# Optimization experiments

Hardware: AMD Instinct MI355X
Metric: run time of the kernel (lower is better)

The kernel has to match this reference:

```python
import jax, jax.numpy as jnp
import numpy as np

EMBED_DIM = 2048
NUM_HEADS = 16
HEAD_DIM = EMBED_DIM // NUM_HEADS
BATCH, SEQ = 4, 4096


def setup_inputs() -> dict:
    key = jax.random.key(0)
    k1, k2, k3, k4 = jax.random.split(key, 4)
    scale = 1.0 / np.sqrt(EMBED_DIM)
    x = jax.random.normal(k1, (BATCH, SEQ, EMBED_DIM), dtype=jnp.float32)
    W_qkv = jax.random.normal(k2, (EMBED_DIM, 3 * EMBED_DIM), dtype=jnp.float32) * scale
    W_out = jax.random.normal(k3, (EMBED_DIM, EMBED_DIM), dtype=jnp.float32) * scale
    b_out = jax.random.normal(k4, (EMBED_DIM,), dtype=jnp.float32) * 0.01
    return {"x": x, "W_qkv": W_qkv, "W_out": W_out, "b_out": b_out}


def reference(x, W_qkv, W_out, b_out):
    b, s, _ = x.shape
    # qkv: (b, s, 3, h, d)
    qkv = (x @ W_qkv).reshape(b, s, 3, NUM_HEADS, HEAD_DIM)
    q, k, v = qkv[:, :, 0], qkv[:, :, 1], qkv[:, :, 2]
    # NOTE: faithful to source — scores mix HEADS per token: (b, s, h, h)
    scores = jnp.einsum('bshd,bsHd->bshH', q, k) / jnp.sqrt(jnp.float32(HEAD_DIM))
    w = jax.nn.softmax(scores, axis=-1)
    attn = jnp.einsum('bshH,bsHd->bshd', w, v).reshape(b, s, EMBED_DIM)
    return attn @ W_out + b_out
```

## Files before the change

### kernel.cpp

```cpp
#include <hip/hip_runtime.h>
#include <hip/hip_bf16.h>
#include <cstdint>


#define TOKENS 16384
#define EMB    2048
#define NQKV   6144

typedef __bf16 bf16x8_t __attribute__((ext_vector_type(8)));
typedef float  f32x4_t  __attribute__((ext_vector_type(4)));

#define GLOAD16(gsrc, ldst)                                                    \
  __builtin_amdgcn_global_load_lds(                                            \
      (const __attribute__((address_space(1))) void*)(uintptr_t)(gsrc),        \
      (__attribute__((address_space(3))) void*)(uint32_t)(uintptr_t)(ldst),    \
      16, 0, 0)

static __device__ __forceinline__ unsigned short f32_to_bf16_bits(float f) {
  union { float f; uint32_t u; } x; x.f = f;
  uint32_t u = x.u;
  u += 0x7fffu + ((u >> 16) & 1u);
  return (unsigned short)(u >> 16);
}

__global__ __launch_bounds__(256) void cvt_f32_bf16(
    const float4* __restrict__ in, ushort4* __restrict__ out, int n4) {
  const int stride = gridDim.x * blockDim.x;
  for (int i = blockIdx.x * blockDim.x + threadIdx.x; i < n4; i += stride) {
    float4 v = in[i];
    ushort4 o;
    o.x = f32_to_bf16_bits(v.x);
    o.y = f32_to_bf16_bits(v.y);
    o.z = f32_to_bf16_bits(v.z);
    o.w = f32_to_bf16_bits(v.w);
    out[i] = o;
  }
}

__global__ __launch_bounds__(256) void transpose_cvt(
    const float* __restrict__ in, unsigned short* __restrict__ out, int R, int C) {
  __shared__ float tile[32][33];
  const int bx = blockIdx.x * 32;
  const int by = blockIdx.y * 32;
  const int tx = threadIdx.x;
  const int ty = threadIdx.y;
#pragma unroll
  for (int j = 0; j < 32; j += 8)
    tile[ty + j][tx] = in[(size_t)(by + ty + j) * C + bx + tx];
  __syncthreads();
#pragma unroll
  for (int j = 0; j < 32; j += 8)
    out[(size_t)(bx + ty + j) * R + by + tx] = f32_to_bf16_bits(tile[tx][ty + j]);
}

template <bool OUT_BF16>
__global__ __launch_bounds__(512, 1) void gemm_bt(
    const unsigned short* __restrict__ A,
    const unsigned short* __restrict__ BT,
    unsigned short* __restrict__ Cb,
    float* __restrict__ Cf,
    const float* __restrict__ bias,
    int M, int N) {
  constexpr int K = 2048;
  constexpr int BK = 64;
  constexpr int NKT = K / BK;
  __shared__ __align__(16) char lds[131072];

  const int nbx = N / 256;
  const int nwg = gridDim.x;
  const int bid = blockIdx.x;
  const int swzb = (bid & 7) * (nwg >> 3) + (bid >> 3);
  const int by = swzb / nbx;
  const int bx = swzb % nbx;

  const int t    = threadIdx.x;
  const int lane = t & 63;
  const int wid  = t >> 6;
  const int wr   = wid >> 2;
  const int wc   = wid & 3;
  const int lr   = lane & 15;
  const int g    = lane >> 4;

  const unsigned short* aSrc = A  + (size_t)by * 256 * K;
  const unsigned short* bSrc = BT + (size_t)bx * 256 * K;

  int aoff[2], boff[2];
#pragma unroll
  for (int i = 0; i < 2; ++i) {
    const int p   = (i * 512 + t) * 16;
    const int lo  = p ^ (((p >> 7) & 7) << 4);
    const int rih = lo >> 7;
    const int kbe = (lo & 127) >> 1;
    aoff[i] = (((rih >> 6) << 7) + (rih & 63)) * K + kbe;
    boff[i] = (((rih >> 5) << 6) + (rih & 31)) * K + kbe;
  }
  const int ldst = wid << 10;

  auto stageA = [&](int h, int k0, char* bufA) {
#pragma unroll
    for (int i = 0; i < 2; ++i)
      GLOAD16(aSrc + aoff[i] + h * (64 * K) + k0, bufA + h * 16384 + i * 8192 + ldst);
  };
  auto stageB = [&](int h, int k0, char* bufB) {
#pragma unroll
    for (int i = 0; i < 2; ++i)
      GLOAD16(bSrc + boff[i] + h * (32 * K) + k0, bufB + h * 16384 + i * 8192 + ldst);
  };

  const int sw   = (lr & 7) << 4;
  const int col0 = (g * 16) ^ sw;
  const int col1 = (64 + g * 16) ^ sw;
  const int aRow = (wr * 64 + lr) * 128;
  const int bRow = (wc * 32 + lr) * 128;

  f32x4_t acc[8][4] = {};
  bf16x8_t av0[4][2], av1[4][2];
  bf16x8_t bv0[2][2], bv1[2][2];

#define LDA_INTO(dst, bufA_, q)                                                \
  {                                                                            \
    const char* _b = (bufA_) + (q) * 16384 + aRow;                             \
    _Pragma("unroll") for (int m2 = 0; m2 < 4; ++m2) {                         \
      dst[m2][0] = *(const bf16x8_t*)(_b + m2 * 2048 + col0);                  \
      dst[m2][1] = *(const bf16x8_t*)(_b + m2 * 2048 + col1);                  \
    }                                                                          \
  }
#define LDB_INTO(dst, bufB_, pair)                                             \
  {                                                                            \
    _Pragma("unroll") for (int e = 0; e < 2; ++e) {                            \
      const int nf = (pair) * 2 + e;                                           \
      const char* _b = (bufB_) + (nf >> 1) * 16384 + (nf & 1) * 2048 + bRow;   \
      dst[e][0] = *(const bf16x8_t*)(_b + col0);                               \
      dst[e][1] = *(const bf16x8_t*)(_b + col1);                               \
    }                                                                          \
  }
#define MFMAQ(AV, BV, Q, PAIR)                                                 \
  _Pragma("unroll") for (int m2 = 0; m2 < 4; ++m2)                             \
  _Pragma("unroll") for (int e = 0; e < 2; ++e)                                \
  _Pragma("unroll") for (int ks = 0; ks < 2; ++ks)                             \
    acc[(Q) * 4 + m2][(PAIR) * 2 + e] = __builtin_amdgcn_mfma_f32_16x16x32_bf16( \
        AV[m2][ks], BV[e][ks], acc[(Q) * 4 + m2][(PAIR) * 2 + e], 0, 0, 0);

#define SBR __builtin_amdgcn_sched_barrier(0)
#define TAIL(NN)                                                               \
  SBR; __builtin_amdgcn_s_barrier();                                           \
  asm volatile("s_waitcnt lgkmcnt(" #NN ")" ::: "memory");                     \
  SBR; __builtin_amdgcn_s_setprio(1);
#define PEND                                                                   \
  __builtin_amdgcn_s_setprio(0); SBR; __builtin_amdgcn_s_barrier();
#define VMC(NN) asm volatile("s_waitcnt vmcnt(" #NN ")" ::: "memory"); SBR;

#define BODY(KT, S1, S2, VM3, VM4, T4)                                         \
  {                                                                            \
    char* cA = lds + ((KT) & 1) * 65536;                                       \
    char* cB = cA + 32768;                                                     \
    char* nA = lds + (((KT) + 1) & 1) * 65536;                                 \
    char* nB = nA + 32768;                                                     \
    const int k2 = ((KT) + 2) * BK;                                            \
      \
    LDB_INTO(bv1, cB, 1); SBR;                                                 \
    TAIL(4);                                                                   \
    MFMAQ(av0, bv0, 0, 0);                                                     \
    LDA_INTO(av1, cA, 1);                                                      \
    PEND;                                                                      \
                               \
    if (S2) { stageA(0, k2, cA); } SBR;                                        \
    TAIL(8);                                                                   \
    MFMAQ(av0, bv1, 0, 1);                                                     \
    PEND;                                                                      \
                                         \
    VMC(VM3);                                                                  \
    if (S2) { stageB(0, k2, cB); } SBR;                                        \
    TAIL(0);                                                                   \
    MFMAQ(av1, bv1, 1, 1);                                                     \
    PEND;                                                                      \
                             \
    VMC(VM4);                                                                  \
    if (S2) { stageA(1, k2, cA); stageB(1, k2, cB); } SBR;                     \
    if (S1) { LDA_INTO(av0, nA, 0); } SBR;                                     \
    TAIL(T4);                                                                  \
    MFMAQ(av1, bv0, 1, 0);                                                     \
    if (S1) { LDB_INTO(bv0, nB, 0); }                                          \
    PEND;                                                                      \
  }

  {
    char* b0A = lds;
    char* b0B = lds + 32768;
    char* b1A = lds + 65536;
    char* b1B = b1A + 32768;
    stageA(0, 0, b0A); stageA(1, 0, b0A);
    stageB(0, 0, b0B); stageB(1, 0, b0B);
    stageA(0, BK, b1A);
    stageB(0, BK, b1B);
    stageA(1, BK, b1A);
    stageB(1, BK, b1B);
    asm volatile("s_waitcnt vmcnt(8)" ::: "memory");
    __builtin_amdgcn_s_barrier();
    LDA_INTO(av0, b0A, 0);
    LDB_INTO(bv0, b0B, 0);
    SBR;
  }

  for (int kt = 0; kt < NKT - 2; ++kt) {
    BODY(kt, 1, 1, 6, 4, 8);
  }
  BODY(NKT - 2, 1, 0, 4, 0, 8);
  BODY(NKT - 1, 0, 0, 0, 0, 0);

  const int rbase = by * 256 + wr * 128 + g * 4;
  const int cbase = bx * 256 + wc * 64 + lr;
#pragma unroll
  for (int m = 0; m < 8; ++m) {
#pragma unroll
    for (int nf = 0; nf < 4; ++nf) {
      const int col = cbase + nf * 16;
#pragma unroll
      for (int j = 0; j < 4; ++j) {
        const size_t off = (size_t)(rbase + (m >> 2) * 64 + (m & 3) * 16 + j) * N + col;
        if constexpr (OUT_BF16) {
          Cb[off] = f32_to_bf16_bits(acc[m][nf][j]);
        } else {
          Cf[off] = acc[m][nf][j] + bias[col];
        }
      }
    }
  }
#undef LDA_INTO
#undef LDB_INTO
#undef MFMAQ
#undef SBR
#undef TAIL
#undef PEND
#undef VMC
#undef BODY
}

__global__ __launch_bounds__(256) void attn_heads(
    const unsigned short* __restrict__ qkv,
    unsigned short* __restrict__ attn) {
  __shared__ __align__(16) unsigned short sQKV[NQKV];
  __shared__ float sW[16][16];

  const int t = threadIdx.x;
  const size_t qbase = (size_t)blockIdx.x * NQKV;

  const uint4* gp = (const uint4*)(qkv + qbase);
  uint4* l = (uint4*)sQKV;
#pragma unroll
  for (int i = 0; i < 3; ++i) {
    const int idx = i * 256 + t;
    int dst = idx;
    if (idx >= 256 && idx < 512) {
      const int r = (idx - 256) >> 4;
      const int c = idx & 15;
      dst = 256 + r * 16 + (c ^ (r & 7));
    }
    l[dst] = gp[idx];
  }
  __syncthreads();

  const int h = t >> 4;
  const int H = t & 15;
  const bf16x8_t* q8 = (const bf16x8_t*)sQKV + h * 16;
  const bf16x8_t* k8 = (const bf16x8_t*)sQKV + 256;
  float s = 0.f;
#pragma unroll
  for (int d8 = 0; d8 < 16; ++d8) {
    bf16x8_t qv = q8[d8];
    bf16x8_t kv = k8[H * 16 + (d8 ^ (H & 7))];
#pragma unroll
    for (int j = 0; j < 8; ++j)
      s = fmaf((float)qv[j], (float)kv[j], s);
  }
  s *= 0.08838834764831843f;

  float mx = s;
#pragma unroll
  for (int o = 8; o; o >>= 1) mx = fmaxf(mx, __shfl_xor(mx, o));
  const float e = __expf(s - mx);
  float sum = e;
#pragma unroll
  for (int o = 8; o; o >>= 1) sum += __shfl_xor(sum, o);
  sW[h][H] = e / sum;
  __syncthreads();

  const int d0c = t & 15;
  const bf16x8_t* v8 = (const bf16x8_t*)sQKV + 512;
  float accv[8] = {};
#pragma unroll
  for (int j = 0; j < 16; ++j) {
    const float w = sW[h][j];
    const bf16x8_t vv = v8[j * 16 + d0c];
#pragma unroll
    for (int jj = 0; jj < 8; ++jj)
      accv[jj] = fmaf(w, (float)vv[jj], accv[jj]);
  }
  bf16x8_t o;
#pragma unroll
  for (int jj = 0; jj < 8; ++jj) o[jj] = (__bf16)accv[jj];
  *(bf16x8_t*)(attn + (size_t)blockIdx.x * EMB + h * 128 + d0c * 8) = o;
}

extern "C" void kernel_launch(void* const* d_in, const int* in_sizes, int n_in,
                              void* d_out, int out_size, void* d_ws, size_t ws_size,
                              hipStream_t stream) {
  const float* x    = (const float*)d_in[0];
  const float* Wqkv = (const float*)d_in[1];
  const float* Wout = (const float*)d_in[2];
  const float* bout = (const float*)d_in[3];
  float* out = (float*)d_out;

  unsigned short* xb    = (unsigned short*)d_ws;
  unsigned short* wqkvT = xb    + (size_t)33554432;
  unsigned short* woutT = wqkvT + (size_t)12582912;
  unsigned short* qkv   = woutT + (size_t)4194304;
  unsigned short* attn  = qkv   + (size_t)100663296;

  cvt_f32_bf16<<<2048, 256, 0, stream>>>((const float4*)x, (ushort4*)xb, 33554432 / 4);
  transpose_cvt<<<dim3(6144 / 32, 2048 / 32), dim3(32, 8), 0, stream>>>(Wqkv, wqkvT, 2048, 6144);
  transpose_cvt<<<dim3(2048 / 32, 2048 / 32), dim3(32, 8), 0, stream>>>(Wout, woutT, 2048, 2048);
  gemm_bt<true><<<(16384 / 256) * (6144 / 256), 512, 0, stream>>>(
      xb, wqkvT, qkv, nullptr, nullptr, 16384, 6144);
  attn_heads<<<TOKENS, 256, 0, stream>>>(qkv, attn);
  gemm_bt<false><<<(16384 / 256) * (2048 / 256), 512, 0, stream>>>(
      attn, woutT, nullptr, out, bout, 16384, 2048);
}
```

Measured before the change: 627.8 us.

## Restructure GEMM main loop into two-phase schedule with fewer barriers

Replaces the four-phase per-k-tile body, which had interleaved LDS fragment loads, global-to-LDS stages and a barrier pair per phase, with a two-phase body. Each tile now loads all A/B fragments up front, stages the next tiles' chunks in a new order (A half of k+1 delayed, B and A0 of k+2 after the first barrier), and runs two MFMA groups per phase. The goal is to cut barrier and waitcnt overhead, at the cost of less overlap between LDS reads and MFMA and higher register pressure from holding all fragments at once.

```diff
diff --git a/kernel.cpp b/kernel.cpp
--- a/kernel.cpp
+++ b/kernel.cpp
@@ -142,46 +142,33 @@
         AV[m2][ks], BV[e][ks], acc[(Q) * 4 + m2][(PAIR) * 2 + e], 0, 0, 0);
 
 #define SBR __builtin_amdgcn_sched_barrier(0)
-#define TAIL(NN)                                                               \
-  SBR; __builtin_amdgcn_s_barrier();                                           \
-  asm volatile("s_waitcnt lgkmcnt(" #NN ")" ::: "memory");                     \
-  SBR; __builtin_amdgcn_s_setprio(1);
-#define PEND                                                                   \
-  __builtin_amdgcn_s_setprio(0); SBR; __builtin_amdgcn_s_barrier();
-#define VMC(NN) asm volatile("s_waitcnt vmcnt(" #NN ")" ::: "memory"); SBR;
-
-#define BODY(KT, S1, S2, VM3, VM4, T4)                                         \
+
+#define BODY(KT, S1, S2, VMN)                                                  \
   {                                                                            \
     char* cA = lds + ((KT) & 1) * 65536;                                       \
     char* cB = cA + 32768;                                                     \
     char* nA = lds + (((KT) + 1) & 1) * 65536;                                 \
-    char* nB = nA + 32768;                                                     \
-    const int k2 = ((KT) + 2) * BK;                                            \
+    const int k1 = ((KT) + 1) * BK, k2 = ((KT) + 2) * BK;                      \
+                  \
+    LDA_INTO(av0, cA, 0);                                                      \
+    LDB_INTO(bv0, cB, 0);                                                      \
+    LDB_INTO(bv1, cB, 1);                                                      \
+    LDA_INTO(av1, cA, 1); SBR;                                                 \
+    if (S1) { stageA(1, k1, nA); } SBR;                                        \
+    asm volatile("s_waitcnt lgkmcnt(0)" ::: "memory"); SBR;                    \
+    __builtin_amdgcn_s_setprio(1);                                             \
+    MFMAQ(av0, bv0, 0, 0);                                                     \
+    MFMAQ(av0, bv1, 0, 1);                                                     \
+    __builtin_amdgcn_s_setprio(0); SBR;                                        \
+    __builtin_amdgcn_s_barrier();                                              \
       \
-    LDB_INTO(bv1, cB, 1); SBR;                                                 \
-    TAIL(4);                                                                   \
-    MFMAQ(av0, bv0, 0, 0);                                                     \
-    LDA_INTO(av1, cA, 1);                                                      \
-    PEND;                                                                      \
-                               \
-    if (S2) { stageA(0, k2, cA); } SBR;                                        \
-    TAIL(8);                                                                   \
-    MFMAQ(av0, bv1, 0, 1);                                                     \
-    PEND;                                                                      \
-                                         \
-    VMC(VM3);                                                                  \
-    if (S2) { stageB(0, k2, cB); } SBR;                                        \
-    TAIL(0);                                                                   \
+    if (S2) { stageB(0, k2, cB); stageB(1, k2, cB); stageA(0, k2, cA); } SBR;  \
+    __builtin_amdgcn_s_setprio(1);                                             \
     MFMAQ(av1, bv1, 1, 1);                                                     \
-    PEND;                                                                      \
-                             \
-    VMC(VM4);                                                                  \
-    if (S2) { stageA(1, k2, cA); stageB(1, k2, cB); } SBR;                     \
-    if (S1) { LDA_INTO(av0, nA, 0); } SBR;                                     \
-    TAIL(T4);                                                                  \
     MFMAQ(av1, bv0, 1, 0);                                                     \
-    if (S1) { LDB_INTO(bv0, nB, 0); }                                          \
-    PEND;                                                                      \
+    __builtin_amdgcn_s_setprio(0); SBR;                                        \
+    asm volatile("s_waitcnt vmcnt(" #VMN ")" ::: "memory"); SBR;               \
+    __builtin_amdgcn_s_barrier();                                              \
   }
 
   {
@@ -191,22 +178,17 @@
     char* b1B = b1A + 32768;
     stageA(0, 0, b0A); stageA(1, 0, b0A);
     stageB(0, 0, b0B); stageB(1, 0, b0B);
+    stageB(0, BK, b1B); stageB(1, BK, b1B);
     stageA(0, BK, b1A);
-    stageB(0, BK, b1B);
-    stageA(1, BK, b1A);
-    stageB(1, BK, b1B);
-    asm volatile("s_waitcnt vmcnt(8)" ::: "memory");
+    asm volatile("s_waitcnt vmcnt(6)" ::: "memory");
     __builtin_amdgcn_s_barrier();
-    LDA_INTO(av0, b0A, 0);
-    LDB_INTO(bv0, b0B, 0);
-    SBR;
   }
 
   for (int kt = 0; kt < NKT - 2; ++kt) {
-    BODY(kt, 1, 1, 6, 4, 8);
-  }
-  BODY(NKT - 2, 1, 0, 4, 0, 8);
-  BODY(NKT - 1, 0, 0, 0, 0, 0);
+    BODY(kt, 1, 1, 6);
+  }
+  BODY(NKT - 2, 1, 0, 0);
+  BODY(NKT - 1, 0, 0, 0);
 
   const int rbase = by * 256 + wr * 128 + g * 4;
   const int cbase = bx * 256 + wc * 64 + lr;
@@ -230,9 +212,6 @@
 #undef LDB_INTO
 #undef MFMAQ
 #undef SBR
-#undef TAIL
-#undef PEND
-#undef VMC
 #undef BODY
 }
 
```

Result: no change. 616.5 us (-1.8%).
